# Optimization experiments

Measured on AMD Instinct MI355X. Metric: run time of the kernel, lower is better.

The kernel has to match this reference:

```python
import jax, jax.numpy as jnp
import numpy as np


def setup_inputs() -> dict:
    key = jax.random.key(0)
    kq, ks, kr, kx, ky = jax.random.split(key, 5)
    B, C, H, W, K = 2, 64, 128, 256, 32
    Q = jax.random.normal(kq, (B, C, H, W), dtype=jnp.float32)
    S = jax.random.normal(ks, (B, C, H, W), dtype=jnp.float32)
    R = jax.random.normal(kr, (B, C, H, W), dtype=jnp.float32)
    Pos_x = jax.random.randint(kx, (H * W, K), 0, H, dtype=jnp.int64 if jax.config.jax_enable_x64 else jnp.int32)
    Pos_y = jax.random.randint(ky, (H * W, K), 0, W, dtype=jnp.int64 if jax.config.jax_enable_x64 else jnp.int32)
    return {"Q": Q, "S": S, "R": R, "Pos_x": Pos_x, "Pos_y": Pos_y}


def reference(Q, S, R, Pos_x, Pos_y):
    B, C, H, W = Q.shape
    N = H * W
    px = Pos_x.reshape(-1)  # [N*K]
    py = Pos_y.reshape(-1)
    K = px.shape[0] // N
    # Gather keys/values at candidate positions: [B, C, N*K] -> [B, C, N, K]
    Key = S[:, :, px, py].reshape(B, C, N, K)
    Value = R[:, :, px, py].reshape(B, C, N, K)
    # Queries: [B, N, C]
    Qf = Q.reshape(B, C, N).transpose(0, 2, 1)
    # Per-pixel scores over K candidates (NO 1/sqrt(d) scaling, as in original)
    score = jnp.einsum('bnc,bcnk->bnk', Qf, Key)
    attn = jax.nn.softmax(score, axis=-1)
    # Attention-weighted sum of values: [B, N, C]
    out = jnp.einsum('bnk,bcnk->bnc', attn, Value)
    return out.reshape(B, H, W, C).transpose(0, 3, 1, 2)
```

## Files before the change

kernel.cpp:

```cpp
#include <hip/hip_runtime.h>
#include <hip/hip_fp16.h>

constexpr int B = 2, C = 64, H = 128, W = 256, N = H * W, K = 32;

typedef _Float16 hf2 __attribute__((ext_vector_type(2)));

template <int CTRL>
__device__ __forceinline__ float dppf(float x) {
    int i = __builtin_bit_cast(int, x);
    int r = __builtin_amdgcn_update_dpp(i, i, CTRL, 0xF, 0xF, false);
    return __builtin_bit_cast(float, r);
}

__global__ __launch_bounds__(256) void fepam_prep(
    const float* __restrict__ Q, const float* __restrict__ S,
    const float* __restrict__ R,
    const int* __restrict__ Px, const int* __restrict__ Py,
    __half* __restrict__ Qt, __half* __restrict__ St, __half* __restrict__ Rt,
    unsigned short* __restrict__ Idx) {
    const int n0 = blockIdx.x * 64;
    const int b  = blockIdx.y;
    const int z  = blockIdx.z;

    if (z == 3) {
        if (b) return;
#pragma unroll
        for (int t = 0; t < 8; ++t) {
            const int e  = threadIdx.x + 256 * t;
            const int nl = e >> 5, k = e & 31;
            const int n  = n0 + nl;
            const int idx = Px[(size_t)n * K + k] * W + Py[(size_t)n * K + k];
            Idx[(size_t)n * K + (k & 7) * 4 + (k >> 3)] = (unsigned short)idx;
        }
        return;
    }

    __shared__ float tile[C][65];
    const float* src = (z == 0 ? S : (z == 1 ? R : Q)) + (size_t)b * C * N;
    __half2* d2 = (__half2*)((z == 0 ? St : (z == 1 ? Rt : Qt)) +
                             (size_t)b * N * C);
    {
        const int j = threadIdx.x & 63, c0 = threadIdx.x >> 6;
        const float* s = src + n0 + j;
#pragma unroll
        for (int r = 0; r < 16; ++r) {
            int c = c0 + r * 4;
            tile[c][j] = s[(size_t)c * N];
        }
    }
    __syncthreads();
    {
        const int c2 = threadIdx.x & 31, j0 = threadIdx.x >> 5;
#pragma unroll
        for (int r = 0; r < 8; ++r) {
            int j = j0 + 8 * r;
            d2[(size_t)(n0 + j) * 32 + c2] =
                __floats2half2_rn(tile[2 * c2][j], tile[2 * c2 + 1][j]);
        }
    }
}

__global__ __launch_bounds__(512, 8) void fepam_attn(
    const __half* __restrict__ Qt, const unsigned short* __restrict__ Idx,
    const __half* __restrict__ St, const __half* __restrict__ Rt,
    float* __restrict__ Out) {
    __shared__ __align__(16) float ot[64][66];

    const int tid  = threadIdx.x;
    const int lane = tid & 63;
    const int wave = tid >> 6;
    const int bx   = blockIdx.x;
    const int b    = bx & 1;
    const int n0   = (bx >> 1) * 64;

    const int c_oct = lane & 7;
    const int k_loc = lane >> 3;
    const bool hi8  = (lane & 8)  != 0;
    const bool hi16 = (lane & 16) != 0;
    const bool hi32 = (lane & 32) != 0;

    const __half* Qtb = Qt + (size_t)b * N * C;
    const __half* Stb = St + (size_t)b * N * C;
    const __half* Rtb = Rt + (size_t)b * N * C;

#pragma unroll 2
    for (int p = 0; p < 8; ++p) {
        const int j = wave * 8 + p;
        const int n = n0 + j;

        const float4 qraw = *(const float4*)(Qtb + (size_t)n * C + c_oct * 8);
        const ushort4 iv = *(const ushort4*)(Idx + (size_t)n * K + k_loc * 4);
        const int idxg[4] = {iv.x, iv.y, iv.z, iv.w};

        float s[4];
#pragma unroll
        for (int g = 0; g < 4; ++g) {
            const float4 kraw =
                *(const float4*)(Stb + ((size_t)idxg[g] << 6) + c_oct * 8);
            const hf2* k2 = (const hf2*)&kraw;
            const hf2* q2 = (const hf2*)&qraw;
            float acc = 0.f;
#pragma unroll
            for (int u = 0; u < 4; ++u)
                acc = __builtin_amdgcn_fdot2(k2[u], q2[u], acc, false);
            s[g] = acc;
        }
#pragma unroll
        for (int g = 0; g < 4; ++g) {
            s[g] += dppf<0xB1>(s[g]);
            s[g] += dppf<0x4E>(s[g]);
            s[g] += dppf<0x141>(s[g]);
        }

        float m = fmaxf(fmaxf(s[0], s[1]), fmaxf(s[2], s[3]));
        m = fmaxf(m, dppf<0x128>(m));
        m = fmaxf(m, __shfl_xor(m, 16));
        m = fmaxf(m, __shfl_xor(m, 32));
        float e0 = __expf(s[0] - m), e1 = __expf(s[1] - m);
        float e2 = __expf(s[2] - m), e3 = __expf(s[3] - m);
        float l = (e0 + e1) + (e2 + e3);
        l += dppf<0x128>(l);
        l += __shfl_xor(l, 16);
        l += __shfl_xor(l, 32);
        const float inv = 1.0f / l;
        const float a[4] = {e0 * inv, e1 * inv, e2 * inv, e3 * inv};

        float acc[8] = {0, 0, 0, 0, 0, 0, 0, 0};
#pragma unroll
        for (int g = 0; g < 4; ++g) {
            const float4 vraw =
                *(const float4*)(Rtb + ((size_t)idxg[g] << 6) + c_oct * 8);
            const __half2* v2 = (const __half2*)&vraw;
            const float ag = a[g];
#pragma unroll
            for (int u = 0; u < 4; ++u) {
                const float2 vf = __half22float2(v2[u]);
                acc[2 * u]     = fmaf(ag, vf.x, acc[2 * u]);
                acc[2 * u + 1] = fmaf(ag, vf.y, acc[2 * u + 1]);
            }
        }

        float r4[4];
#pragma unroll
        for (int i = 0; i < 4; ++i) {
            const float send = hi8 ? acc[i] : acc[4 + i];
            const float recv = dppf<0x128>(send);
            r4[i] = (hi8 ? acc[4 + i] : acc[i]) + recv;
        }
        float r2[2];
#pragma unroll
        for (int i = 0; i < 2; ++i) {
            const float send = hi16 ? r4[i] : r4[2 + i];
            const float recv = __shfl_xor(send, 16);
            r2[i] = (hi16 ? r4[2 + i] : r4[i]) + recv;
        }
        {
            const float send = hi32 ? r2[0] : r2[1];
            const float recv = __shfl_xor(send, 32);
            const float r1   = (hi32 ? r2[1] : r2[0]) + recv;
            const int c = c_oct * 8 + (hi8 ? 4 : 0) + (hi16 ? 2 : 0) + (hi32 ? 1 : 0);
            ot[j][c] = r1;
        }
    }
    __syncthreads();

    {
        const int j = tid & 63, c0 = tid >> 6;
        float* od = Out + (size_t)b * C * N + n0 + j;
#pragma unroll
        for (int r = 0; r < 8; ++r) {
            int c = c0 + r * 8;
            od[(size_t)c * N] = ot[j][c];
        }
    }
}

extern "C" void kernel_launch(void* const* d_in, const int* in_sizes, int n_in,
                              void* d_out, int out_size, void* d_ws, size_t ws_size,
                              hipStream_t stream) {
    const float* Q  = (const float*)d_in[0];
    const float* S  = (const float*)d_in[1];
    const float* R  = (const float*)d_in[2];
    const int*   Px = (const int*)d_in[3];
    const int*   Py = (const int*)d_in[4];
    float* Out = (float*)d_out;

    __half* St = (__half*)d_ws;
    __half* Rt = St + (size_t)B * N * C;
    __half* Qt = Rt + (size_t)B * N * C;
    unsigned short* Idx = (unsigned short*)(Qt + (size_t)B * N * C);

    dim3 pgrid(N / 64, B, 4);
    fepam_prep<<<pgrid, 256, 0, stream>>>(Q, S, R, Px, Py, Qt, St, Rt, Idx);

    dim3 agrid(N / 64 * B);
    fepam_attn<<<agrid, 512, 0, stream>>>(Qt, Idx, St, Rt, Out);
}
```

Measured before the change: 155.2 us.

## Split fused attention kernel into separate score and value-gather kernels

Splits the single attention kernel into a scores/softmax kernel that writes fp16 attention weights to workspace and a value kernel that reads them and gathers R. The aim is to let each kernel keep only one gathered table (S or R) hot in cache and to lower register pressure per kernel. The cost is an extra launch, an extra round trip of the N*K attention array through memory, and fp16 rounding of the weights. The ot tile for 32 pixels is still written as ot[j][c] and read back correctly within 32 rows.

```diff
diff --git a/kernel.cpp b/kernel.cpp
--- a/kernel.cpp
+++ b/kernel.cpp
@@ -60,36 +60,29 @@
     }
 }
 
-__global__ __launch_bounds__(512, 8) void fepam_attn(
+__global__ __launch_bounds__(256, 6) void fepam_scores(
     const __half* __restrict__ Qt, const unsigned short* __restrict__ Idx,
-    const __half* __restrict__ St, const __half* __restrict__ Rt,
-    float* __restrict__ Out) {
-    __shared__ __align__(16) float ot[64][66];
-
+    const __half* __restrict__ St, __half* __restrict__ Attn) {
     const int tid  = threadIdx.x;
     const int lane = tid & 63;
     const int wave = tid >> 6;
     const int bx   = blockIdx.x;
     const int b    = bx & 1;
-    const int n0   = (bx >> 1) * 64;
+    const int n0   = (bx >> 1) * 32;
 
     const int c_oct = lane & 7;
     const int k_loc = lane >> 3;
-    const bool hi8  = (lane & 8)  != 0;
-    const bool hi16 = (lane & 16) != 0;
-    const bool hi32 = (lane & 32) != 0;
 
     const __half* Qtb = Qt + (size_t)b * N * C;
     const __half* Stb = St + (size_t)b * N * C;
-    const __half* Rtb = Rt + (size_t)b * N * C;
-
-#pragma unroll 2
+    __half* AttnB = Attn + (size_t)b * N * K;
+
+#pragma unroll
     for (int p = 0; p < 8; ++p) {
-        const int j = wave * 8 + p;
-        const int n = n0 + j;
-
+        const int n = n0 + wave * 8 + p;
+
+        const ushort4 iv = *(const ushort4*)(Idx + (size_t)n * K + k_loc * 4);
         const float4 qraw = *(const float4*)(Qtb + (size_t)n * C + c_oct * 8);
-        const ushort4 iv = *(const ushort4*)(Idx + (size_t)n * K + k_loc * 4);
         const int idxg[4] = {iv.x, iv.y, iv.z, iv.w};
 
         float s[4];
@@ -123,7 +116,51 @@
         l += __shfl_xor(l, 16);
         l += __shfl_xor(l, 32);
         const float inv = 1.0f / l;
-        const float a[4] = {e0 * inv, e1 * inv, e2 * inv, e3 * inv};
+
+        if (c_oct == 0) {
+            ushort4 av;
+            av.x = __half_as_ushort(__float2half_rn(e0 * inv));
+            av.y = __half_as_ushort(__float2half_rn(e1 * inv));
+            av.z = __half_as_ushort(__float2half_rn(e2 * inv));
+            av.w = __half_as_ushort(__float2half_rn(e3 * inv));
+            *(ushort4*)(AttnB + (size_t)n * K + k_loc * 4) = av;
+        }
+    }
+}
+
+__global__ __launch_bounds__(256, 6) void fepam_values(
+    const unsigned short* __restrict__ Idx, const __half* __restrict__ Attn,
+    const __half* __restrict__ Rt, float* __restrict__ Out) {
+    __shared__ __align__(16) float ot[32][66];
+
+    const int tid  = threadIdx.x;
+    const int lane = tid & 63;
+    const int wave = tid >> 6;
+    const int bx   = blockIdx.x;
+    const int b    = bx & 1;
+    const int n0   = (bx >> 1) * 32;
+
+    const int c_oct = lane & 7;
+    const int k_loc = lane >> 3;
+    const bool hi8  = (lane & 8)  != 0;
+    const bool hi16 = (lane & 16) != 0;
+    const bool hi32 = (lane & 32) != 0;
+
+    const __half* Rtb = Rt + (size_t)b * N * C;
+    const __half* AttnB = Attn + (size_t)b * N * K;
+
+#pragma unroll
+    for (int p = 0; p < 8; ++p) {
+        const int j = wave * 8 + p;
+        const int n = n0 + j;
+
+        const ushort4 iv = *(const ushort4*)(Idx + (size_t)n * K + k_loc * 4);
+        const ushort4 av = *(const ushort4*)(AttnB + (size_t)n * K + k_loc * 4);
+        const int idxg[4] = {iv.x, iv.y, iv.z, iv.w};
+        const float a[4] = {__half2float(__ushort_as_half(av.x)),
+                            __half2float(__ushort_as_half(av.y)),
+                            __half2float(__ushort_as_half(av.z)),
+                            __half2float(__ushort_as_half(av.w))};
 
         float acc[8] = {0, 0, 0, 0, 0, 0, 0, 0};
 #pragma unroll
@@ -131,12 +168,11 @@
             const float4 vraw =
                 *(const float4*)(Rtb + ((size_t)idxg[g] << 6) + c_oct * 8);
             const __half2* v2 = (const __half2*)&vraw;
-            const float ag = a[g];
 #pragma unroll
             for (int u = 0; u < 4; ++u) {
                 const float2 vf = __half22float2(v2[u]);
-                acc[2 * u]     = fmaf(ag, vf.x, acc[2 * u]);
-                acc[2 * u + 1] = fmaf(ag, vf.y, acc[2 * u + 1]);
+                acc[2 * u]     = fmaf(a[g], vf.x, acc[2 * u]);
+                acc[2 * u + 1] = fmaf(a[g], vf.y, acc[2 * u + 1]);
             }
         }
 
@@ -165,7 +201,7 @@
     __syncthreads();
 
     {
-        const int j = tid & 63, c0 = tid >> 6;
+        const int j = tid & 31, c0 = tid >> 5;
         float* od = Out + (size_t)b * C * N + n0 + j;
 #pragma unroll
         for (int r = 0; r < 8; ++r) {
@@ -189,10 +225,12 @@
     __half* Rt = St + (size_t)B * N * C;
     __half* Qt = Rt + (size_t)B * N * C;
     unsigned short* Idx = (unsigned short*)(Qt + (size_t)B * N * C);
+    __half* Attn = (__half*)(Idx + (size_t)N * K);
 
     dim3 pgrid(N / 64, B, 4);
     fepam_prep<<<pgrid, 256, 0, stream>>>(Q, S, R, Px, Py, Qt, St, Rt, Idx);
 
-    dim3 agrid(N / 64 * B);
-    fepam_attn<<<agrid, 512, 0, stream>>>(Qt, Idx, St, Rt, Out);
-}
+    dim3 ggrid(N / 32 * B);
+    fepam_scores<<<ggrid, 256, 0, stream>>>(Qt, Idx, St, Attn);
+    fepam_values<<<ggrid, 256, 0, stream>>>(Idx, Attn, Rt, Out);
+}
```

Result: faster. 139.9 us (-9.8%).
